# Performance work log

Hardware: AMD Instinct MI355X
Metric: run time of the kernel (lower is better)

Reference implementation:

```python
import jax, jax.numpy as jnp
import numpy as np
import math

V, T, E, H, L = 32000, 1024, 1024, 16, 6
B = 2
D = E // H
F = 4 * E


def setup_inputs() -> dict:
    key = jax.random.key(0)
    ks = jax.random.split(key, 12)
    s = 0.02
    rn = lambda k, shape: jax.random.normal(k, shape, jnp.float32) * s
    return dict(
        idx=jax.random.randint(ks[0], (B, T), 0, V),
        tok_w=rn(ks[1], (V, E)),
        pos_w=rn(ks[2], (T, E)),
        ln1_g=jnp.ones((L, E)), ln1_b=jnp.zeros((L, E)),
        wq=rn(ks[3], (L, E, E)), wk=rn(ks[4], (L, E, E)), wv=rn(ks[5], (L, E, E)),
        wp=rn(ks[6], (L, E, E)), bp=jnp.zeros((L, E)),
        ln2_g=jnp.ones((L, E)), ln2_b=jnp.zeros((L, E)),
        w1=rn(ks[7], (L, E, F)), b1=jnp.zeros((L, F)),
        w2=rn(ks[8], (L, F, E)), b2=jnp.zeros((L, E)),
        lnf_g=jnp.ones((E,)), lnf_b=jnp.zeros((E,)),
        wlm=rn(ks[9], (E, V)), blm=jnp.zeros((V,)),
    )


def _layernorm(x, g, b, eps=1e-5):
    m = jnp.mean(x, axis=-1, keepdims=True)
    v = jnp.var(x, axis=-1, keepdims=True)
    return (x - m) * jax.lax.rsqrt(v + eps) * g + b


def _forward(idx, tok_w, pos_w, ln1_g, ln1_b, wq, wk, wv, wp, bp,
             ln2_g, ln2_b, w1, b1, w2, b2, lnf_g, lnf_b, wlm, blm):
    Bx, Tx = idx.shape
    x = tok_w[idx] + pos_w[jnp.arange(Tx)][None, :, :]  # [B,T,E]
    causal = jnp.tril(jnp.ones((Tx, Tx), dtype=bool))
    scale = 1.0 / math.sqrt(D)
    for l in range(L):
        h = _layernorm(x, ln1_g[l], ln1_b[l])
        q = (h @ wq[l]).reshape(Bx, Tx, H, D).transpose(0, 2, 1, 3)  # [B,H,T,D]
        k = (h @ wk[l]).reshape(Bx, Tx, H, D).transpose(0, 2, 1, 3)
        v = (h @ wv[l]).reshape(Bx, Tx, H, D).transpose(0, 2, 1, 3)
        att = jnp.einsum('bhtd,bhsd->bhts', q, k) * scale  # [B,H,T,T]
        att = jnp.where(causal, att, -jnp.inf)
        att = jax.nn.softmax(att, axis=-1)
        y = jnp.einsum('bhts,bhsd->bhtd', att, v)
        y = y.transpose(0, 2, 1, 3).reshape(Bx, Tx, E)
        x = x + y @ wp[l] + bp[l]
        h2 = _layernorm(x, ln2_g[l], ln2_b[l])
        ff = jax.nn.gelu(h2 @ w1[l] + b1[l], approximate=False) @ w2[l] + b2[l]
        x = x + ff
    x = _layernorm(x, lnf_g, lnf_b)
    return x @ wlm + blm  # logits [B,T,V]


def reference(idx, tok_w, pos_w, ln1_g, ln1_b, wq, wk, wv, wp, bp,
              ln2_g, ln2_b, w1, b1, w2, b2, lnf_g, lnf_b, wlm, blm):
    return _forward(idx, tok_w, pos_w, ln1_g, ln1_b, wq, wk, wv, wp, bp,
                    ln2_g, ln2_b, w1, b1, w2, b2, lnf_g, lnf_b, wlm, blm)
```

## Files before the change

kernel.cpp:

```cpp
#include <hip/hip_runtime.h>

#define T_SEQ   1024
#define E_DIM   1024
#define H_HEADS 16
#define D_HEAD  64
#define L_LAYERS 6
#define B_BATCH 2
#define F_DIM   4096
#define V_VOCAB 32000

typedef float f32x4 __attribute__((ext_vector_type(4)));
typedef short short8 __attribute__((ext_vector_type(8)));

__device__ __forceinline__ unsigned short f2bf(float f) {
  union { float f; unsigned int u; } v; v.f = f;
  unsigned int r = v.u + 0x7fffu + ((v.u >> 16) & 1u);
  return (unsigned short)(r >> 16);
}

#define GLDS16(gp, lp) __builtin_amdgcn_global_load_lds( \
    (const __attribute__((address_space(1))) void*)(gp), \
    (__attribute__((address_space(3))) void*)(lp), 16, 0, 0)

__global__ void embed_kernel(const int* __restrict__ idx, const float* __restrict__ tok,
                             const float* __restrict__ pos, float* __restrict__ x) {
  int i = blockIdx.x * 256 + threadIdx.x;
  int bt = i >> 8;
  int e4 = i & 255;
  int t  = bt & (T_SEQ - 1);
  int tokid = idx[bt];
  f32x4 a = *(const f32x4*)(tok + (size_t)tokid * E_DIM + e4 * 4);
  f32x4 p = *(const f32x4*)(pos + (size_t)t * E_DIM + e4 * 4);
  *(f32x4*)(x + (size_t)bt * E_DIM + e4 * 4) = a + p;
}

__device__ __forceinline__ void ln_body(const float* __restrict__ x,
    const float* __restrict__ g, const float* __restrict__ b,
    unsigned short* __restrict__ out, int row) {
  int tid = threadIdx.x;
  const float* xr = x + (size_t)row * E_DIM;
  f32x4 v = *(const f32x4*)(xr + tid * 4);
  float s  = v[0] + v[1] + v[2] + v[3];
  float s2 = v[0]*v[0] + v[1]*v[1] + v[2]*v[2] + v[3]*v[3];
  #pragma unroll
  for (int off = 32; off > 0; off >>= 1) {
    s  += __shfl_xor(s,  off);
    s2 += __shfl_xor(s2, off);
  }
  __shared__ float red[2][4];
  int wave = tid >> 6;
  if ((tid & 63) == 0) { red[0][wave] = s; red[1][wave] = s2; }
  __syncthreads();
  s  = red[0][0] + red[0][1] + red[0][2] + red[0][3];
  s2 = red[1][0] + red[1][1] + red[1][2] + red[1][3];
  float mean = s * (1.0f / E_DIM);
  float var  = s2 * (1.0f / E_DIM) - mean * mean;
  float rstd = rsqrtf(var + 1e-5f);
  f32x4 gv = *(const f32x4*)(g + tid * 4);
  f32x4 bv = *(const f32x4*)(b + tid * 4);
  ushort4 o;
  o.x = f2bf((v[0] - mean) * rstd * gv[0] + bv[0]);
  o.y = f2bf((v[1] - mean) * rstd * gv[1] + bv[1]);
  o.z = f2bf((v[2] - mean) * rstd * gv[2] + bv[2]);
  o.w = f2bf((v[3] - mean) * rstd * gv[3] + bv[3]);
  *(ushort4*)(out + (size_t)row * E_DIM + tid * 4) = o;
}

__global__ void ln_kernel(const float* __restrict__ x, const float* __restrict__ g,
                          const float* __restrict__ b, unsigned short* __restrict__ out) {
  ln_body(x, g, b, out, blockIdx.x);
}

__device__ __forceinline__ void wtrans_body(const float* __restrict__ W,
    unsigned short* __restrict__ Wt, int K, int N, int bx, int by) {
  __shared__ float tile[64][65];
  const int n0 = bx * 64, k0 = by * 64;
  const int tr  = threadIdx.x >> 4;
  const int tc4 = (threadIdx.x & 15) * 4;
  #pragma unroll
  for (int p = 0; p < 4; ++p) {
    f32x4 v = *(const f32x4*)(W + (size_t)(k0 + p * 16 + tr) * N + n0 + tc4);
    tile[p * 16 + tr][tc4 + 0] = v[0];
    tile[p * 16 + tr][tc4 + 1] = v[1];
    tile[p * 16 + tr][tc4 + 2] = v[2];
    tile[p * 16 + tr][tc4 + 3] = v[3];
  }
  __syncthreads();
  #pragma unroll
  for (int p = 0; p < 4; ++p) {
    int n = p * 16 + tr;
    ushort4 o;
    o.x = f2bf(tile[tc4 + 0][n]);
    o.y = f2bf(tile[tc4 + 1][n]);
    o.z = f2bf(tile[tc4 + 2][n]);
    o.w = f2bf(tile[tc4 + 3][n]);
    *(ushort4*)(Wt + (size_t)(n0 + n) * K + k0 + tc4) = o;
  }
}

__global__ __launch_bounds__(256) void wtrans6ln_kernel(const float* __restrict__ wq,
    const float* __restrict__ wk, const float* __restrict__ wv, const float* __restrict__ wp,
    const float* __restrict__ w1, const float* __restrict__ w2,
    const float* __restrict__ lng, const float* __restrict__ lnb,
    const float* __restrict__ x, unsigned short* __restrict__ wtb,
    unsigned short* __restrict__ hb) {
  const size_t EE = (size_t)E_DIM * E_DIM;
  const size_t EF = (size_t)E_DIM * F_DIM;
  const int id = blockIdx.x;
  if (id < 1024) {
    const int z = id >> 8, r = id & 255;
    const float* W = z == 0 ? wq : (z == 1 ? wk : (z == 2 ? wv : wp));
    wtrans_body(W, wtb + z * EE, E_DIM, E_DIM, r & 15, r >> 4);
  } else if (id < 2048) {
    const int r = id - 1024;
    wtrans_body(w1, wtb + 4 * EE, E_DIM, F_DIM, r & 63, r >> 6);
  } else if (id < 3072) {
    const int r = id - 2048;
    wtrans_body(w2, wtb + 4 * EE + EF, F_DIM, E_DIM, r & 15, r >> 4);
  } else {
    ln_body(x, lng, lnb, hb, id - 3072);
  }
}

__global__ __launch_bounds__(256) void wtransv_ln_kernel(const float* __restrict__ wlm,
    const float* __restrict__ lng, const float* __restrict__ lnb,
    const float* __restrict__ x, unsigned short* __restrict__ wtb,
    unsigned short* __restrict__ hb) {
  const int id = blockIdx.x;
  if (id < 8000) wtrans_body(wlm, wtb, E_DIM, V_VOCAB, id % 500, id / 500);
  else           ln_body(x, lng, lnb, hb, id - 8000);
}

__global__ __launch_bounds__(512) void attn_mfma_kernel(
    const unsigned short* __restrict__ qk, const unsigned short* __restrict__ vt,
    unsigned short* __restrict__ y) {
  __shared__ __align__(16) char smem[2 * 16384 + 8 * 1280 + 512];
  const int tid  = threadIdx.x;
  const int lane = tid & 63;
  const int wave = tid >> 6;
  const int wl = wave & 3;
  const int g  = wave >> 2;
  const int qx = blockIdx.x;
  const int h  = blockIdx.y & (H_HEADS - 1);
  const int b  = blockIdx.y >> 4;
  const int qt = b ? (15 - qx) : qx;
  const int r0 = qt * 64 + wl * 16;
  const size_t RS = 2 * E_DIM;
  const unsigned short* q  = qk + (size_t)b * T_SEQ * RS + (size_t)h * D_HEAD;
  const unsigned short* k  = q + E_DIM;
  const unsigned short* vb = vt + (size_t)(b * H_HEADS + h) * D_HEAD * T_SEQ;
  const size_t ybase = (size_t)b * T_SEQ * E_DIM + (size_t)h * D_HEAD;
  const int fr = lane & 15, fg = lane >> 4;
  const int srow = lane >> 3;
  const int ssw  = ((lane & 7) * 16) ^ (srow << 4);
  char* pb = smem + 32768 + wave * 1280;
  float* mlb = (float*)(smem + 32768 + 10240);

  short8 aq[2];
  #pragma unroll
  for (int c = 0; c < 2; ++c)
    aq[c] = *(const short8*)(q + (size_t)(r0 + fr) * RS + c * 32 + fg * 8);

  f32x4 oacc[4];
  #pragma unroll
  for (int cg = 0; cg < 4; ++cg) oacc[cg] = (f32x4){0.f, 0.f, 0.f, 0.f};
  float m_ = -1e30f, l_ = 0.0f;

  auto stage = [&](int t) {
    const int j0 = t * 64;
    char* Kd = smem + (t & 1) * 16384;
    GLDS16((const char*)k  + (size_t)(j0 + wave * 8 + srow) * RS * 2 + ssw,
           Kd + wave * 1024);
    GLDS16((const char*)vb + ((size_t)(wave * 8 + srow) * T_SEQ + j0) * 2 + ssw,
           Kd + 8192 + wave * 1024);
  };

  stage(0);
  for (int t = 0; t <= qt; ++t) {
    __builtin_amdgcn_sched_barrier(0);
    __builtin_amdgcn_s_barrier();
    if (t < qt) stage(t + 1);
    __builtin_amdgcn_sched_barrier(0);
    if (t < qt) asm volatile("s_waitcnt vmcnt(2)" ::: "memory");
    else        asm volatile("s_waitcnt vmcnt(0)" ::: "memory");
    __builtin_amdgcn_sched_barrier(0);
    __builtin_amdgcn_s_barrier();
    __builtin_amdgcn_sched_barrier(0);
    const char* Kl = smem + (t & 1) * 16384;
    const char* Vl = Kl + 8192;
    const int j0 = t * 64;
    if (!(t == qt && g == 1 && wl < 2)) {
      f32x4 st[2];
      #pragma unroll
      for (int cc = 0; cc < 2; ++cc) {
        const int kloc = g * 32 + cc * 16 + fr;
        const char* kb = Kl + kloc * 128;
        const int sw = (kloc & 7) << 4;
        short8 ka0 = *(const short8*)(kb + ((fg * 16) ^ sw));
        short8 ka1 = *(const short8*)(kb + ((64 + fg * 16) ^ sw));
        f32x4 z = (f32x4){0.f, 0.f, 0.f, 0.f};
        z = __builtin_amdgcn_mfma_f32_16x16x32_bf16(ka0, aq[0], z, 0, 0, 0);
        z = __builtin_amdgcn_mfma_f32_16x16x32_bf16(ka1, aq[1], z, 0, 0, 0);
        st[cc] = z;
      }
      const int qg = r0 + fr;
      float pv[2][4];
      float mx = -1e30f;
      #pragma unroll
      for (int cc = 0; cc < 2; ++cc)
        #pragma unroll
        for (int r = 0; r < 4; ++r) {
          const int kj = j0 + g * 32 + cc * 16 + fg * 4 + r;
          float val = (kj <= qg) ? st[cc][r] * 0.125f : -1e30f;
          pv[cc][r] = val;
          mx = fmaxf(mx, val);
        }
      mx = fmaxf(mx, __shfl_xor(mx, 16));
      mx = fmaxf(mx, __shfl_xor(mx, 32));
      const float mn = fmaxf(m_, mx);
      const float cfs = __expf(m_ - mn);
      float ls = 0.0f;
      #pragma unroll
      for (int cc = 0; cc < 2; ++cc) {
        ushort4 o;
        float e0 = pv[cc][0] > -1e29f ? __expf(pv[cc][0] - mn) : 0.0f;
        float e1 = pv[cc][1] > -1e29f ? __expf(pv[cc][1] - mn) : 0.0f;
        float e2 = pv[cc][2] > -1e29f ? __expf(pv[cc][2] - mn) : 0.0f;
        float e3 = pv[cc][3] > -1e29f ? __expf(pv[cc][3] - mn) : 0.0f;
        ls += (e0 + e1) + (e2 + e3);
        o.x = f2bf(e0); o.y = f2bf(e1); o.z = f2bf(e2); o.w = f2bf(e3);
        *(ushort4*)(pb + fr * 80 + cc * 32 + fg * 8) = o;
      }
      ls += __shfl_xor(ls, 16);
      ls += __shfl_xor(ls, 32);
      l_ = l_ * cfs + ls;
      m_ = mn;
      float cfO[4];
      #pragma unroll
      for (int r = 0; r < 4; ++r) cfO[r] = __shfl(cfs, (lane & 48) | (fg * 4 + r));
      asm volatile("s_waitcnt lgkmcnt(0)" ::: "memory");
      __builtin_amdgcn_sched_barrier(0);
      short8 pa = *(const short8*)(pb + fr * 80 + fg * 16);
      __builtin_amdgcn_s_setprio(1);
      #pragma unroll
      for (int cg = 0; cg < 4; ++cg) {
        const int d = cg * 16 + fr;
        short8 bv = *(const short8*)(Vl + d * 128 + ((g * 64 + fg * 16) ^ ((d & 7) << 4)));
        #pragma unroll
        for (int r = 0; r < 4; ++r) oacc[cg][r] *= cfO[r];
        oacc[cg] = __builtin_amdgcn_mfma_f32_16x16x32_bf16(pa, bv, oacc[cg], 0, 0, 0);
      }
      __builtin_amdgcn_s_setprio(0);
    }
  }
  __syncthreads();
  float* obuf = (float*)smem;
  if (g == 1) {
    #pragma unroll
    for (int cg = 0; cg < 4; ++cg)
      #pragma unroll
      for (int r = 0; r < 4; ++r)
        obuf[wl * 1024 + (fg * 4 + r) * 64 + cg * 16 + fr] = oacc[cg][r];
    if (fg == 0) { mlb[(wl * 16 + fr) * 2] = m_; mlb[(wl * 16 + fr) * 2 + 1] = l_; }
  }
  __syncthreads();
  if (g == 0) {
    const float m1 = mlb[(wl * 16 + fr) * 2];
    const float l1 = mlb[(wl * 16 + fr) * 2 + 1];
    const float m  = fmaxf(m_, m1);
    const float c0 = __expf(m_ - m), c1 = __expf(m1 - m);
    const float li = 1.0f / (l_ * c0 + l1 * c1);
    float c0O[4], c1O[4], liO[4];
    #pragma unroll
    for (int r = 0; r < 4; ++r) {
      const int src = (lane & 48) | (fg * 4 + r);
      c0O[r] = __shfl(c0, src); c1O[r] = __shfl(c1, src); liO[r] = __shfl(li, src);
    }
    #pragma unroll
    for (int cg = 0; cg < 4; ++cg)
      #pragma unroll
      for (int r = 0; r < 4; ++r) {
        const float o1 = obuf[wl * 1024 + (fg * 4 + r) * 64 + cg * 16 + fr];
        const float val = (oacc[cg][r] * c0O[r] + o1 * c1O[r]) * liO[r];
        y[ybase + (size_t)(r0 + fg * 4 + r) * E_DIM + cg * 16 + fr] = f2bf(val);
      }
  }
}

template<int BM, int BN, bool HAS_BIAS, bool GELU_ACT, bool HAS_RES, int OMODE>
__global__ __launch_bounds__(256) void gemm_bt_kernel(
    const unsigned short* __restrict__ A, const unsigned short* __restrict__ Bt,
    const float* __restrict__ bias, const float* __restrict__ res,
    void* __restrict__ out, unsigned short* __restrict__ vt, int M, int N, int K) {
  constexpr int BK = 64;
  constexpr int MR = BM / 32;
  constexpr int NR = BN / 32;
  constexpr int AI = BM / 32;
  constexpr int BI = BN / 32;
  __shared__ __align__(16) char smem[(BM + BN) * BK * 2];
  unsigned short* As = (unsigned short*)smem;
  unsigned short* Bs = (unsigned short*)(smem + (size_t)BM * BK * 2);
  const int tid  = threadIdx.x;
  const int lane = tid & 63;
  const int wave = tid >> 6;
  const int wr = wave >> 1, wc = wave & 1;

  const int mt = M / BM;
  const int q8 = gridDim.x >> 3;
  const int g  = (blockIdx.x & 7) * q8 + (blockIdx.x >> 3);
  const int m0 = (g % mt) * BM, n0 = (g / mt) * BN;

  const int fr = lane & 15, fg = lane >> 4;
  const int lrow = lane >> 3;
  const int scol = ((lane & 7) * 16) ^ (lrow << 4);
  const size_t K2 = (size_t)K * 2;
  const char* aG = (const char*)A  + (size_t)(m0 + wave * 8 + lrow) * K2 + scol;
  const char* bG = (const char*)Bt + (size_t)(n0 + wave * 8 + lrow) * K2 + scol;

  f32x4 acc[MR][NR];
  #pragma unroll
  for (int mi = 0; mi < MR; ++mi)
    #pragma unroll
    for (int ni = 0; ni < NR; ++ni) acc[mi][ni] = (f32x4){0.f, 0.f, 0.f, 0.f};

  for (int k0 = 0; k0 < K; k0 += BK) {
    __syncthreads();
    #pragma unroll
    for (int i = 0; i < AI; ++i)
      GLDS16(aG + (size_t)i * 32 * K2 + (size_t)k0 * 2, (char*)As + wave * 1024 + i * 4096);
    #pragma unroll
    for (int i = 0; i < BI; ++i)
      GLDS16(bG + (size_t)i * 32 * K2 + (size_t)k0 * 2, (char*)Bs + wave * 1024 + i * 4096);
    __syncthreads();

    short8 af[MR][2], bf[NR][2];
    #pragma unroll
    for (int mi = 0; mi < MR; ++mi) {
      const int row = wr * (BM / 2) + mi * 16 + fr;
      #pragma unroll
      for (int kh = 0; kh < 2; ++kh)
        af[mi][kh] = *(const short8*)((const char*)As + row * 128 +
                       ((kh * 64 + fg * 16) ^ ((row & 7) << 4)));
    }
    #pragma unroll
    for (int ni = 0; ni < NR; ++ni) {
      const int row = wc * (BN / 2) + ni * 16 + fr;
      #pragma unroll
      for (int kh = 0; kh < 2; ++kh)
        bf[ni][kh] = *(const short8*)((const char*)Bs + row * 128 +
                       ((kh * 64 + fg * 16) ^ ((row & 7) << 4)));
    }
    #pragma unroll
    for (int mi = 0; mi < MR; ++mi)
      #pragma unroll
      for (int ni = 0; ni < NR; ++ni) {
        acc[mi][ni] = __builtin_amdgcn_mfma_f32_16x16x32_bf16(af[mi][0], bf[ni][0], acc[mi][ni], 0, 0, 0);
        acc[mi][ni] = __builtin_amdgcn_mfma_f32_16x16x32_bf16(af[mi][1], bf[ni][1], acc[mi][ni], 0, 0, 0);
      }
  }

  if (OMODE == 0) {
    __syncthreads();
    float* tw = (float*)(smem + wave * 4352);
    float bv4[NR];
    #pragma unroll
    for (int ni = 0; ni < NR; ++ni)
      bv4[ni] = HAS_BIAS ? bias[n0 + wc * (BN / 2) + ni * 16 + fr] : 0.0f;
    #pragma unroll
    for (int mi = 0; mi < MR; ++mi) {
      #pragma unroll
      for (int ni = 0; ni < NR; ++ni)
        #pragma unroll
        for (int r = 0; r < 4; ++r) {
          float val = acc[mi][ni][r] + bv4[ni];
          if (GELU_ACT) val = 0.5f * val * (1.0f + erff(val * 0.70710678118f));
          tw[(fg * 4 + r) * 68 + ni * 16 + fr] = val;
        }
      asm volatile("s_waitcnt lgkmcnt(0)" ::: "memory");
      __builtin_amdgcn_sched_barrier(0);
      #pragma unroll
      for (int rr = 0; rr < 4; ++rr) {
        const int row = rr * 4 + (lane >> 4);
        const int grow = m0 + wr * (BM / 2) + mi * 16 + row;
        const int gcol = n0 + wc * (BN / 2) + (lane & 15) * 4;
        f32x4 v = *(const f32x4*)&tw[row * 68 + (lane & 15) * 4];
        if (HAS_RES) v += *(const f32x4*)(res + (size_t)grow * N + gcol);
        *(f32x4*)((float*)out + (size_t)grow * N + gcol) = v;
      }
      asm volatile("s_waitcnt lgkmcnt(0)" ::: "memory");
      __builtin_amdgcn_sched_barrier(0);
    }
  } else {
    #pragma unroll
    for (int mi = 0; mi < MR; ++mi)
      #pragma unroll
      for (int ni = 0; ni < NR; ++ni) {
        const int col = n0 + wc * (BN / 2) + ni * 16 + fr;
        float bv = HAS_BIAS ? bias[col] : 0.0f;
        const int rbase = m0 + wr * (BM / 2) + mi * 16 + fg * 4;
        #pragma unroll
        for (int r = 0; r < 4; ++r) {
          float val = acc[mi][ni][r] + bv;
          if (GELU_ACT) val = 0.5f * val * (1.0f + erff(val * 0.70710678118f));
          ((unsigned short*)out)[(size_t)(rbase + r) * N + col] = f2bf(val);
        }
      }
  }
}

template<int OMODE, bool HAS_BIAS, bool GELU_ACT>
__global__ __launch_bounds__(512, 1) void gemm8p2_kernel(
    const unsigned short* __restrict__ A, const unsigned short* __restrict__ Bt,
    const float* __restrict__ bias, void* __restrict__ out,
    unsigned short* __restrict__ vt, int M, int N, int K) {
  __shared__ __align__(16) char lds[98304];
  const int tid  = threadIdx.x;
  const int lane = tid & 63;
  const int wv   = tid >> 6;
  const int wm = wv >> 2, wn = wv & 3;

  const int mt = M >> 7;
  const int q8 = gridDim.x >> 3;
  const int g  = (blockIdx.x & 7) * q8 + (blockIdx.x >> 3);
  const int m0 = (g % mt) * 128, n0 = (g / mt) * 256;

  const int fr = lane & 15, fg = lane >> 4;
  const size_t K2 = (size_t)K * 2;
  const int nIter = K >> 7;

  const int csw0 = (fg * 16) ^ ((fr & 7) << 4);
  const int csw1 = (64 + fg * 16) ^ ((fr & 7) << 4);

  const int sc = (lane * 16) & 127;
  const size_t laneoff = (size_t)(lane >> 3) * K2 + (size_t)(sc ^ ((lane >> 3) << 4));
  const char* Asrc = (const char*)(A + (size_t)m0 * K) + laneoff;
  const char* Bsrc = (const char*)(Bt + (size_t)n0 * K) + laneoff;
  const int arow_wv = (wv >> 2) * 64 + (wv & 3) * 8;
  const int brow_wv = (wv >> 2) * 64 + (wv & 3) * 8;

  f32x4 acc[4][4];
  #pragma unroll
  for (int i = 0; i < 4; ++i)
    #pragma unroll
    for (int j = 0; j < 4; ++j) acc[i][j] = (f32x4){0.f, 0.f, 0.f, 0.f};

  auto stageA = [&](int b, int c, int kt) {
    GLDS16(Asrc + (size_t)(arow_wv + c * 32) * K2 + (size_t)kt * 128,
           lds + b * 49152 + c * 8192 + wv * 1024);
  };
  auto stageB = [&](int b, int j, int kt) {
    GLDS16(Bsrc + (size_t)((j & 1) * 128 + (j >> 1) * 32 + brow_wv) * K2 + (size_t)kt * 128,
           lds + b * 49152 + 16384 + j * 8192 + wv * 1024);
  };

  stageA(0, 0, 0); stageA(0, 1, 0);
  stageB(0, 0, 0); stageB(0, 1, 0); stageB(0, 2, 0); stageB(0, 3, 0);
  stageA(1, 0, 1); stageB(1, 0, 1); stageB(1, 1, 1);
  __builtin_amdgcn_sched_barrier(0);
  asm volatile("s_waitcnt vmcnt(3)" ::: "memory");
  __builtin_amdgcn_s_barrier();

  for (int i = 0; i < nIter; ++i) {
    const bool last = (i == nIter - 1);
    #pragma unroll
    for (int p = 0; p < 8; ++p) {
      const int b  = p >> 2;
      const int mh = (p >> 1) & 1;
      const int nh = p & 1;
      const char* Ab = lds + b * 49152;
      const char* Bb = Ab + 16384;
      __builtin_amdgcn_sched_barrier(0);
      short8 fa[2][2], fb[2][2];
      #pragma unroll
      for (int j = 0; j < 2; ++j) {
        const int row = mh * 64 + wm * 32 + j * 16 + fr;
        fa[j][0] = *(const short8*)(Ab + row * 128 + csw0);
        fa[j][1] = *(const short8*)(Ab + row * 128 + csw1);
      }
      #pragma unroll
      for (int n = 0; n < 2; ++n) {
        const int row = nh * 128 + (wn >> 1) * 64 + (wn & 1) * 32 + n * 16 + fr;
        fb[n][0] = *(const short8*)(Bb + row * 128 + csw0);
        fb[n][1] = *(const short8*)(Bb + row * 128 + csw1);
      }
      if (p == 0) stageA(1, 1, 2 * i + 1);
      if (p == 1) { stageB(1, 2, 2 * i + 1); stageB(1, 3, 2 * i + 1); }
      if (!last) {
        if (p == 2) stageA(0, 0, 2 * i + 2);
        if (p == 3) { stageB(0, 0, 2 * i + 2); stageB(0, 1, 2 * i + 2); }
        if (p == 4) stageA(0, 1, 2 * i + 2);
        if (p == 5) { stageB(0, 2, 2 * i + 2); stageB(0, 3, 2 * i + 2); }
        if (p == 6) stageA(1, 0, 2 * i + 3);
        if (p == 7) { stageB(1, 0, 2 * i + 3); stageB(1, 1, 2 * i + 3); }
      }
      __builtin_amdgcn_sched_barrier(0);
      __builtin_amdgcn_s_barrier();
      __builtin_amdgcn_sched_barrier(0);
      __builtin_amdgcn_s_setprio(1);
      #pragma unroll
      for (int j = 0; j < 2; ++j)
        #pragma unroll
        for (int n = 0; n < 2; ++n) {
          acc[mh * 2 + j][nh * 2 + n] = __builtin_amdgcn_mfma_f32_16x16x32_bf16(
              fa[j][0], fb[n][0], acc[mh * 2 + j][nh * 2 + n], 0, 0, 0);
          acc[mh * 2 + j][nh * 2 + n] = __builtin_amdgcn_mfma_f32_16x16x32_bf16(
              fa[j][1], fb[n][1], acc[mh * 2 + j][nh * 2 + n], 0, 0, 0);
        }
      __builtin_amdgcn_s_setprio(0);
      __builtin_amdgcn_sched_barrier(0);
      if (p == 3) {
        if (!last) asm volatile("s_waitcnt vmcnt(3)" ::: "memory");
        else       asm volatile("s_waitcnt vmcnt(0)" ::: "memory");
      }
      if (p == 7 && !last)
        asm volatile("s_waitcnt vmcnt(3)" ::: "memory");
      __builtin_amdgcn_s_barrier();
    }
  }

  if (OMODE == 1) {
    unsigned short* tw = (unsigned short*)(lds + wv * 2176);
    float bv4[4];
    #pragma unroll
    for (int ni = 0; ni < 4; ++ni)
      bv4[ni] = HAS_BIAS ? bias[n0 + wn * 64 + ni * 16 + fr] : 0.0f;
    #pragma unroll
    for (int mi = 0; mi < 4; ++mi) {
      #pragma unroll
      for (int ni = 0; ni < 4; ++ni)
        #pragma unroll
        for (int r = 0; r < 4; ++r) {
          float val = acc[mi][ni][r] + bv4[ni];
          if (GELU_ACT) val = 0.5f * val * (1.0f + erff(val * 0.70710678118f));
          tw[(fg * 4 + r) * 68 + ni * 16 + fr] = f2bf(val);
        }
      asm volatile("s_waitcnt lgkmcnt(0)" ::: "memory");
      __builtin_amdgcn_sched_barrier(0);
      #pragma unroll
      for (int rr = 0; rr < 4; ++rr) {
        const int row = rr * 4 + (lane >> 4);
        const int grow = m0 + wm * 64 + mi * 16 + row;
        const int gcol = n0 + wn * 64 + (lane & 15) * 4;
        ushort4 v = *(const ushort4*)&tw[row * 68 + (lane & 15) * 4];
        *(ushort4*)((unsigned short*)out + (size_t)grow * N + gcol) = v;
      }
      asm volatile("s_waitcnt lgkmcnt(0)" ::: "memory");
      __builtin_amdgcn_sched_barrier(0);
    }
  } else {
    #pragma unroll
    for (int mi = 0; mi < 4; ++mi) {
      #pragma unroll
      for (int ni = 0; ni < 4; ++ni) {
        const int col = n0 + wn * 64 + ni * 16 + fr;
        float bv = HAS_BIAS ? bias[col] : 0.0f;
        const int rbase = m0 + wm * 64 + mi * 16 + fg * 4;
        float vals[4];
        #pragma unroll
        for (int r = 0; r < 4; ++r) vals[r] = acc[mi][ni][r] + bv;
        if (col < 2 * E_DIM) {
          #pragma unroll
          for (int r = 0; r < 4; ++r)
            ((unsigned short*)out)[(size_t)(rbase + r) * 2 * E_DIM + col] = f2bf(vals[r]);
        } else {
          const int c2 = col - 2 * E_DIM;
          const int hh = c2 >> 6, d = c2 & 63;
          const int bb = rbase >> 10, t0 = rbase & (T_SEQ - 1);
          ushort4 o;
          o.x = f2bf(vals[0]); o.y = f2bf(vals[1]);
          o.z = f2bf(vals[2]); o.w = f2bf(vals[3]);
          *(ushort4*)(vt + ((size_t)(bb * H_HEADS + hh) * D_HEAD + d) * T_SEQ + t0) = o;
        }
      }
    }
  }
}

__global__ __launch_bounds__(512, 1) void gemm8p_kernel(
    const unsigned short* __restrict__ A, const unsigned short* __restrict__ Bt,
    const float* __restrict__ bias, float* __restrict__ out, int M, int N, int K) {
  __shared__ __align__(16) char lds[131072];
  const int tid  = threadIdx.x;
  const int lane = tid & 63;
  const int wv   = tid >> 6;
  const int wm = wv >> 2, wn = wv & 3;

  const int mt = M >> 8;
  const int q8 = gridDim.x >> 3;
  const int g  = (blockIdx.x & 7) * q8 + (blockIdx.x >> 3);
  const int m0 = (g % mt) * 256, n0 = (g / mt) * 256;

  const int fr = lane & 15, fg = lane >> 4;
  const size_t K2 = (size_t)K * 2;
  const int nIter = K >> 7;

  const int csw0 = (fg * 16) ^ ((fr & 7) << 4);
  const int csw1 = (64 + fg * 16) ^ ((fr & 7) << 4);

  const int sc = (lane * 16) & 127;
  const size_t laneoff = (size_t)(lane >> 3) * K2 + (size_t)(sc ^ ((lane >> 3) << 4));
  const char* Asrc = (const char*)(A + (size_t)m0 * K) + (size_t)(wv * 8) * K2 + laneoff;
  const char* Bsrc = (const char*)(Bt + (size_t)n0 * K) + laneoff;

  f32x4 acc[8][4];
  #pragma unroll
  for (int i = 0; i < 8; ++i)
    #pragma unroll
    for (int j = 0; j < 4; ++j) acc[i][j] = (f32x4){0.f, 0.f, 0.f, 0.f};

  auto stageA = [&](int b, int q, int kt) {
    GLDS16(Asrc + (size_t)(q * 64) * K2 + (size_t)kt * 128,
           lds + b * 65536 + q * 8192 + wv * 1024);
  };
  auto stageB = [&](int b, int j, int o, int kt) {
    const int gw = j * 64 + wv * 8;
    const int rw = ((gw >> 5) << 6) + (gw & 31) + o * 32;
    GLDS16(Bsrc + (size_t)rw * K2 + (size_t)kt * 128,
           lds + b * 65536 + 32768 + rw * 128);
  };

  stageA(0, 0, 0); stageA(0, 2, 0);
  stageB(0, 0, 0, 0); stageB(0, 1, 0, 0);
  stageA(0, 1, 0); stageA(0, 3, 0);
  stageB(0, 0, 1, 0); stageB(0, 1, 1, 0);
  stageA(1, 0, 1); stageA(1, 2, 1);
  stageB(1, 0, 0, 1); stageB(1, 1, 0, 1);
  __builtin_amdgcn_sched_barrier(0);
  asm volatile("s_waitcnt vmcnt(4)" ::: "memory");
  __builtin_amdgcn_s_barrier();

  for (int i = 0; i < nIter; ++i) {
    const bool last = (i == nIter - 1);
    #pragma unroll
    for (int p = 0; p < 8; ++p) {
      const int b  = p >> 2;
      const int mh = (p & 3) >> 1;
      const int nh = p & 1;
      const char* Ab = lds + b * 65536;
      const char* Bb = Ab + 32768;
      __builtin_amdgcn_sched_barrier(0);
      short8 fa[4][2], fb[2][2];
      #pragma unroll
      for (int j = 0; j < 4; ++j) {
        const int row = wm * 128 + mh * 64 + j * 16 + fr;
        fa[j][0] = *(const short8*)(Ab + row * 128 + csw0);
        fa[j][1] = *(const short8*)(Ab + row * 128 + csw1);
      }
      #pragma unroll
      for (int n = 0; n < 2; ++n) {
        const int row = wn * 64 + nh * 32 + n * 16 + fr;
        fb[n][0] = *(const short8*)(Bb + row * 128 + csw0);
        fb[n][1] = *(const short8*)(Bb + row * 128 + csw1);
      }
      if (p == 0) { stageA(1, 1, 2 * i + 1); stageA(1, 3, 2 * i + 1); }
      if (p == 1) { stageB(1, 0, 1, 2 * i + 1); stageB(1, 1, 1, 2 * i + 1); }
      if (!last) {
        if (p == 2) { stageA(0, 0, 2 * i + 2); stageA(0, 2, 2 * i + 2); }
        if (p == 3) { stageB(0, 0, 0, 2 * i + 2); stageB(0, 1, 0, 2 * i + 2); }
        if (p == 4) { stageA(0, 1, 2 * i + 2); stageA(0, 3, 2 * i + 2); }
        if (p == 5) { stageB(0, 0, 1, 2 * i + 2); stageB(0, 1, 1, 2 * i + 2); }
        if (p == 6) { stageA(1, 0, 2 * i + 3); stageA(1, 2, 2 * i + 3); }
        if (p == 7) { stageB(1, 0, 0, 2 * i + 3); stageB(1, 1, 0, 2 * i + 3); }
      }
      __builtin_amdgcn_sched_barrier(0);
      __builtin_amdgcn_s_barrier();
      __builtin_amdgcn_sched_barrier(0);
      __builtin_amdgcn_s_setprio(1);
      #pragma unroll
      for (int j = 0; j < 4; ++j)
        #pragma unroll
        for (int n = 0; n < 2; ++n) {
          acc[mh * 4 + j][nh * 2 + n] = __builtin_amdgcn_mfma_f32_16x16x32_bf16(
              fa[j][0], fb[n][0], acc[mh * 4 + j][nh * 2 + n], 0, 0, 0);
          acc[mh * 4 + j][nh * 2 + n] = __builtin_amdgcn_mfma_f32_16x16x32_bf16(
              fa[j][1], fb[n][1], acc[mh * 4 + j][nh * 2 + n], 0, 0, 0);
        }
      __builtin_amdgcn_s_setprio(0);
      __builtin_amdgcn_sched_barrier(0);
      if (p == 3) {
        if (!last) asm volatile("s_waitcnt vmcnt(4)" ::: "memory");
        else       asm volatile("s_waitcnt vmcnt(0)" ::: "memory");
      }
      if (p == 7 && !last)
        asm volatile("s_waitcnt vmcnt(4)" ::: "memory");
      __builtin_amdgcn_s_barrier();
    }
  }

  float* tw = (float*)(lds + wv * 4352);
  float bv4[4];
  #pragma unroll
  for (int ni = 0; ni < 4; ++ni) bv4[ni] = bias[n0 + wn * 64 + ni * 16 + fr];
  #pragma unroll
  for (int mi = 0; mi < 8; ++mi) {
    #pragma unroll
    for (int ni = 0; ni < 4; ++ni)
      #pragma unroll
      for (int r = 0; r < 4; ++r)
        tw[(fg * 4 + r) * 68 + ni * 16 + fr] = acc[mi][ni][r] + bv4[ni];
    asm volatile("s_waitcnt lgkmcnt(0)" ::: "memory");
    __builtin_amdgcn_sched_barrier(0);
    #pragma unroll
    for (int rr = 0; rr < 4; ++rr) {
      const int row = rr * 4 + (lane >> 4);
      const int grow = m0 + wm * 128 + mi * 16 + row;
      const int gcol = n0 + wn * 64 + (lane & 15) * 4;
      f32x4 v = *(const f32x4*)&tw[row * 68 + (lane & 15) * 4];
      *(f32x4*)(out + (size_t)grow * N + gcol) = v;
    }
    asm volatile("s_waitcnt lgkmcnt(0)" ::: "memory");
    __builtin_amdgcn_sched_barrier(0);
  }
}

extern "C" void kernel_launch(void* const* d_in, const int* in_sizes, int n_in,
                              void* d_out, int out_size, void* d_ws, size_t ws_size,
                              hipStream_t stream) {
  const int*   idx   = (const int*)  d_in[0];
  const float* tok_w = (const float*)d_in[1];
  const float* pos_w = (const float*)d_in[2];
  const float* ln1_g = (const float*)d_in[3];
  const float* ln1_b = (const float*)d_in[4];
  const float* wq    = (const float*)d_in[5];
  const float* wk    = (const float*)d_in[6];
  const float* wv    = (const float*)d_in[7];
  const float* wp    = (const float*)d_in[8];
  const float* bp    = (const float*)d_in[9];
  const float* ln2_g = (const float*)d_in[10];
  const float* ln2_b = (const float*)d_in[11];
  const float* w1    = (const float*)d_in[12];
  const float* b1    = (const float*)d_in[13];
  const float* w2    = (const float*)d_in[14];
  const float* b2    = (const float*)d_in[15];
  const float* lnf_g = (const float*)d_in[16];
  const float* lnf_b = (const float*)d_in[17];
  const float* wlm   = (const float*)d_in[18];
  const float* blm   = (const float*)d_in[19];

  const int M = B_BATCH * T_SEQ;
  const size_t EE = (size_t)E_DIM * E_DIM;
  const size_t EF = (size_t)E_DIM * F_DIM;
  char* p = (char*)d_ws;
  float* x            = (float*)p;          p += (size_t)M * E_DIM * 4;
  unsigned short* hb  = (unsigned short*)p; p += (size_t)M * E_DIM * 2;
  unsigned short* qkb = (unsigned short*)p; p += (size_t)M * 2 * E_DIM * 2;
  unsigned short* vtb = (unsigned short*)p; p += (size_t)M * E_DIM * 2;
  unsigned short* yb  = (unsigned short*)p; p += (size_t)M * E_DIM * 2;
  unsigned short* tb  = (unsigned short*)p; p += (size_t)M * F_DIM * 2;
  unsigned short* wtb = (unsigned short*)p; p += (size_t)V_VOCAB * E_DIM * 2;

  embed_kernel<<<M * E_DIM / 4 / 256, 256, 0, stream>>>(idx, tok_w, pos_w, x);

  for (int l = 0; l < L_LAYERS; ++l) {
    wtrans6ln_kernel<<<5120, 256, 0, stream>>>(
        wq + l * EE, wk + l * EE, wv + l * EE, wp + l * EE,
        w1 + l * EF, w2 + l * EF,
        ln1_g + (size_t)l * E_DIM, ln1_b + (size_t)l * E_DIM, x, wtb, hb);
    gemm8p2_kernel<2, false, false>
        <<<(M / 128) * (3 * E_DIM / 256), 512, 0, stream>>>(
        hb, wtb, nullptr, qkb, vtb, M, 3 * E_DIM, E_DIM);
    attn_mfma_kernel<<<dim3(16, B_BATCH * H_HEADS), 512, 0, stream>>>(qkb, vtb, yb);
    gemm_bt_kernel<64, 128, true, false, true, 0>
        <<<(M / 64) * (E_DIM / 128), 256, 0, stream>>>(
        yb, wtb + 3 * EE, bp + (size_t)l * E_DIM, x, x, nullptr, M, E_DIM, E_DIM);
    ln_kernel<<<M, 256, 0, stream>>>(x, ln2_g + (size_t)l * E_DIM, ln2_b + (size_t)l * E_DIM, hb);
    gemm8p2_kernel<1, true, true>
        <<<(M / 128) * (F_DIM / 256), 512, 0, stream>>>(
        hb, wtb + 4 * EE, b1 + (size_t)l * F_DIM, tb, nullptr, M, F_DIM, E_DIM);
    gemm_bt_kernel<64, 128, true, false, true, 0>
        <<<(M / 64) * (E_DIM / 128), 256, 0, stream>>>(
        tb, wtb + 4 * EE + EF, b2 + (size_t)l * E_DIM, x, x, nullptr, M, E_DIM, F_DIM);
  }
  wtransv_ln_kernel<<<10048, 256, 0, stream>>>(wlm, lnf_g, lnf_b, x, wtb, hb);
  gemm8p_kernel<<<(M / 256) * (V_VOCAB / 256), 512, 0, stream>>>(
      hb, wtb, blm, (float*)d_out, M, V_VOCAB, E_DIM);
}
```

Baseline: 1.292 ms.

## Make LM-head GEMM persistent with cross-tile prefetch and direct epilogue stores

Launches the vocab-projection GEMM with a fixed 256-block persistent grid. Each block walks its XCD-local tiles with stride 32 and prefetches the next tile's first K-slices during the last iteration of the current tile, so the pipeline does not drain and refill between tiles. Because LDS is still holding the prefetched data, the epilogue now writes bias-added accumulators straight to global memory instead of staging them through LDS. That risks less coalesced stores on the large logits output.

```diff
diff --git a/kernel.cpp b/kernel.cpp
--- a/kernel.cpp
+++ b/kernel.cpp
@@ -584,23 +584,34 @@
   const int lane = tid & 63;
   const int wv   = tid >> 6;
   const int wm = wv >> 2, wn = wv & 3;
-
-  const int mt = M >> 8;
-  const int q8 = gridDim.x >> 3;
-  const int g  = (blockIdx.x & 7) * q8 + (blockIdx.x >> 3);
-  const int m0 = (g % mt) * 256, n0 = (g / mt) * 256;
-
   const int fr = lane & 15, fg = lane >> 4;
   const size_t K2 = (size_t)K * 2;
   const int nIter = K >> 7;
+  const int mt = M >> 8;
+  const int perX = (mt * (N >> 8)) >> 3;
+  const int xcd = blockIdx.x & 7, local = blockIdx.x >> 3;
 
   const int csw0 = (fg * 16) ^ ((fr & 7) << 4);
   const int csw1 = (64 + fg * 16) ^ ((fr & 7) << 4);
-
   const int sc = (lane * 16) & 127;
   const size_t laneoff = (size_t)(lane >> 3) * K2 + (size_t)(sc ^ ((lane >> 3) << 4));
-  const char* Asrc = (const char*)(A + (size_t)m0 * K) + (size_t)(wv * 8) * K2 + laneoff;
-  const char* Bsrc = (const char*)(Bt + (size_t)n0 * K) + laneoff;
+
+  auto srcA = [&](int g) {
+    return (const char*)(A + (size_t)((g % mt) * 256) * K) + (size_t)(wv * 8) * K2 + laneoff;
+  };
+  auto srcB = [&](int g) {
+    return (const char*)(Bt + (size_t)((g / mt) * 256) * K) + laneoff;
+  };
+  auto stageA = [&](const char* S, int b, int q, int kt) {
+    GLDS16(S + (size_t)(q * 64) * K2 + (size_t)kt * 128,
+           lds + b * 65536 + q * 8192 + wv * 1024);
+  };
+  auto stageB = [&](const char* S, int b, int j, int o, int kt) {
+    const int gw = j * 64 + wv * 8;
+    const int rw = ((gw >> 5) << 6) + (gw & 31) + o * 32;
+    GLDS16(S + (size_t)rw * K2 + (size_t)kt * 128,
+           lds + b * 65536 + 32768 + rw * 128);
+  };
 
   f32x4 acc[8][4];
   #pragma unroll
@@ -608,108 +619,105 @@
     #pragma unroll
     for (int j = 0; j < 4; ++j) acc[i][j] = (f32x4){0.f, 0.f, 0.f, 0.f};
 
-  auto stageA = [&](int b, int q, int kt) {
-    GLDS16(Asrc + (size_t)(q * 64) * K2 + (size_t)kt * 128,
-           lds + b * 65536 + q * 8192 + wv * 1024);
-  };
-  auto stageB = [&](int b, int j, int o, int kt) {
-    const int gw = j * 64 + wv * 8;
-    const int rw = ((gw >> 5) << 6) + (gw & 31) + o * 32;
-    GLDS16(Bsrc + (size_t)rw * K2 + (size_t)kt * 128,
-           lds + b * 65536 + 32768 + rw * 128);
-  };
-
-  stageA(0, 0, 0); stageA(0, 2, 0);
-  stageB(0, 0, 0, 0); stageB(0, 1, 0, 0);
-  stageA(0, 1, 0); stageA(0, 3, 0);
-  stageB(0, 0, 1, 0); stageB(0, 1, 1, 0);
-  stageA(1, 0, 1); stageA(1, 2, 1);
-  stageB(1, 0, 0, 1); stageB(1, 1, 0, 1);
+  int g = xcd * perX + local;
+  const char* Ac = srcA(g);
+  const char* Bc = srcB(g);
+
+  stageA(Ac, 0, 0, 0); stageA(Ac, 0, 2, 0);
+  stageB(Bc, 0, 0, 0, 0); stageB(Bc, 0, 1, 0, 0);
+  stageA(Ac, 0, 1, 0); stageA(Ac, 0, 3, 0);
+  stageB(Bc, 0, 0, 1, 0); stageB(Bc, 0, 1, 1, 0);
+  stageA(Ac, 1, 0, 1); stageA(Ac, 1, 2, 1);
+  stageB(Bc, 1, 0, 0, 1); stageB(Bc, 1, 1, 0, 1);
   __builtin_amdgcn_sched_barrier(0);
   asm volatile("s_waitcnt vmcnt(4)" ::: "memory");
   __builtin_amdgcn_s_barrier();
 
-  for (int i = 0; i < nIter; ++i) {
-    const bool last = (i == nIter - 1);
-    #pragma unroll
-    for (int p = 0; p < 8; ++p) {
-      const int b  = p >> 2;
-      const int mh = (p & 3) >> 1;
-      const int nh = p & 1;
-      const char* Ab = lds + b * 65536;
-      const char* Bb = Ab + 32768;
-      __builtin_amdgcn_sched_barrier(0);
-      short8 fa[4][2], fb[2][2];
-      #pragma unroll
-      for (int j = 0; j < 4; ++j) {
-        const int row = wm * 128 + mh * 64 + j * 16 + fr;
-        fa[j][0] = *(const short8*)(Ab + row * 128 + csw0);
-        fa[j][1] = *(const short8*)(Ab + row * 128 + csw1);
-      }
-      #pragma unroll
-      for (int n = 0; n < 2; ++n) {
-        const int row = wn * 64 + nh * 32 + n * 16 + fr;
-        fb[n][0] = *(const short8*)(Bb + row * 128 + csw0);
-        fb[n][1] = *(const short8*)(Bb + row * 128 + csw1);
-      }
-      if (p == 0) { stageA(1, 1, 2 * i + 1); stageA(1, 3, 2 * i + 1); }
-      if (p == 1) { stageB(1, 0, 1, 2 * i + 1); stageB(1, 1, 1, 2 * i + 1); }
-      if (!last) {
-        if (p == 2) { stageA(0, 0, 2 * i + 2); stageA(0, 2, 2 * i + 2); }
-        if (p == 3) { stageB(0, 0, 0, 2 * i + 2); stageB(0, 1, 0, 2 * i + 2); }
-        if (p == 4) { stageA(0, 1, 2 * i + 2); stageA(0, 3, 2 * i + 2); }
-        if (p == 5) { stageB(0, 0, 1, 2 * i + 2); stageB(0, 1, 1, 2 * i + 2); }
-        if (p == 6) { stageA(1, 0, 2 * i + 3); stageA(1, 2, 2 * i + 3); }
-        if (p == 7) { stageB(1, 0, 0, 2 * i + 3); stageB(1, 1, 0, 2 * i + 3); }
-      }
-      __builtin_amdgcn_sched_barrier(0);
-      __builtin_amdgcn_s_barrier();
-      __builtin_amdgcn_sched_barrier(0);
-      __builtin_amdgcn_s_setprio(1);
-      #pragma unroll
-      for (int j = 0; j < 4; ++j)
+  for (int w = local; w < perX; w += 32) {
+    const bool finalW = (w + 32 >= perX);
+    const int gN = finalW ? g : (g + 32);
+    const char* An = srcA(gN);
+    const char* Bn = srcB(gN);
+    const int m0 = (g % mt) * 256, n0 = (g / mt) * 256;
+
+    for (int i = 0; i < nIter; ++i) {
+      const bool wrap = (i == nIter - 1);
+      const bool skip = wrap && finalW;
+      const char* Aw = wrap ? An : Ac;
+      const char* Bw = wrap ? Bn : Bc;
+      const int kt2 = wrap ? 0 : (2 * i + 2);
+      const int kt3 = wrap ? 1 : (2 * i + 3);
+      #pragma unroll
+      for (int p = 0; p < 8; ++p) {
+        const int b  = p >> 2;
+        const int mh = (p & 3) >> 1;
+        const int nh = p & 1;
+        const char* Ab = lds + b * 65536;
+        const char* Bb = Ab + 32768;
+        __builtin_amdgcn_sched_barrier(0);
+        short8 fa[4][2], fb[2][2];
+        #pragma unroll
+        for (int j = 0; j < 4; ++j) {
+          const int row = wm * 128 + mh * 64 + j * 16 + fr;
+          fa[j][0] = *(const short8*)(Ab + row * 128 + csw0);
+          fa[j][1] = *(const short8*)(Ab + row * 128 + csw1);
+        }
         #pragma unroll
         for (int n = 0; n < 2; ++n) {
-          acc[mh * 4 + j][nh * 2 + n] = __builtin_amdgcn_mfma_f32_16x16x32_bf16(
-              fa[j][0], fb[n][0], acc[mh * 4 + j][nh * 2 + n], 0, 0, 0);
-          acc[mh * 4 + j][nh * 2 + n] = __builtin_amdgcn_mfma_f32_16x16x32_bf16(
-              fa[j][1], fb[n][1], acc[mh * 4 + j][nh * 2 + n], 0, 0, 0);
-        }
-      __builtin_amdgcn_s_setprio(0);
-      __builtin_amdgcn_sched_barrier(0);
-      if (p == 3) {
-        if (!last) asm volatile("s_waitcnt vmcnt(4)" ::: "memory");
-        else       asm volatile("s_waitcnt vmcnt(0)" ::: "memory");
-      }
-      if (p == 7 && !last)
-        asm volatile("s_waitcnt vmcnt(4)" ::: "memory");
-      __builtin_amdgcn_s_barrier();
-    }
-  }
-
-  float* tw = (float*)(lds + wv * 4352);
-  float bv4[4];
-  #pragma unroll
-  for (int ni = 0; ni < 4; ++ni) bv4[ni] = bias[n0 + wn * 64 + ni * 16 + fr];
-  #pragma unroll
-  for (int mi = 0; mi < 8; ++mi) {
-    #pragma unroll
-    for (int ni = 0; ni < 4; ++ni)
-      #pragma unroll
-      for (int r = 0; r < 4; ++r)
-        tw[(fg * 4 + r) * 68 + ni * 16 + fr] = acc[mi][ni][r] + bv4[ni];
-    asm volatile("s_waitcnt lgkmcnt(0)" ::: "memory");
-    __builtin_amdgcn_sched_barrier(0);
-    #pragma unroll
-    for (int rr = 0; rr < 4; ++rr) {
-      const int row = rr * 4 + (lane >> 4);
-      const int grow = m0 + wm * 128 + mi * 16 + row;
-      const int gcol = n0 + wn * 64 + (lane & 15) * 4;
-      f32x4 v = *(const f32x4*)&tw[row * 68 + (lane & 15) * 4];
-      *(f32x4*)(out + (size_t)grow * N + gcol) = v;
-    }
-    asm volatile("s_waitcnt lgkmcnt(0)" ::: "memory");
-    __builtin_amdgcn_sched_barrier(0);
+          const int row = wn * 64 + nh * 32 + n * 16 + fr;
+          fb[n][0] = *(const short8*)(Bb + row * 128 + csw0);
+          fb[n][1] = *(const short8*)(Bb + row * 128 + csw1);
+        }
+        if (p == 0) { stageA(Ac, 1, 1, 2 * i + 1); stageA(Ac, 1, 3, 2 * i + 1); }
+        if (p == 1) { stageB(Bc, 1, 0, 1, 2 * i + 1); stageB(Bc, 1, 1, 1, 2 * i + 1); }
+        if (!skip) {
+          if (p == 2) { stageA(Aw, 0, 0, kt2); stageA(Aw, 0, 2, kt2); }
+          if (p == 3) { stageB(Bw, 0, 0, 0, kt2); stageB(Bw, 0, 1, 0, kt2); }
+          if (p == 4) { stageA(Aw, 0, 1, kt2); stageA(Aw, 0, 3, kt2); }
+          if (p == 5) { stageB(Bw, 0, 0, 1, kt2); stageB(Bw, 0, 1, 1, kt2); }
+          if (p == 6) { stageA(Aw, 1, 0, kt3); stageA(Aw, 1, 2, kt3); }
+          if (p == 7) { stageB(Bw, 1, 0, 0, kt3); stageB(Bw, 1, 1, 0, kt3); }
+        }
+        __builtin_amdgcn_sched_barrier(0);
+        __builtin_amdgcn_s_barrier();
+        __builtin_amdgcn_sched_barrier(0);
+        __builtin_amdgcn_s_setprio(1);
+        #pragma unroll
+        for (int j = 0; j < 4; ++j)
+          #pragma unroll
+          for (int n = 0; n < 2; ++n) {
+            acc[mh * 4 + j][nh * 2 + n] = __builtin_amdgcn_mfma_f32_16x16x32_bf16(
+                fa[j][0], fb[n][0], acc[mh * 4 + j][nh * 2 + n], 0, 0, 0);
+            acc[mh * 4 + j][nh * 2 + n] = __builtin_amdgcn_mfma_f32_16x16x32_bf16(
+                fa[j][1], fb[n][1], acc[mh * 4 + j][nh * 2 + n], 0, 0, 0);
+          }
+        __builtin_amdgcn_s_setprio(0);
+        __builtin_amdgcn_sched_barrier(0);
+        if (p == 3) {
+          if (!skip) asm volatile("s_waitcnt vmcnt(4)" ::: "memory");
+          else       asm volatile("s_waitcnt vmcnt(0)" ::: "memory");
+        }
+        if (p == 7 && !skip)
+          asm volatile("s_waitcnt vmcnt(4)" ::: "memory");
+        __builtin_amdgcn_s_barrier();
+      }
+    }
+
+    #pragma unroll
+    for (int mi = 0; mi < 8; ++mi) {
+      #pragma unroll
+      for (int ni = 0; ni < 4; ++ni) {
+        const int col = n0 + wn * 64 + ni * 16 + fr;
+        const float bv = bias[col];
+        #pragma unroll
+        for (int r = 0; r < 4; ++r) {
+          const int row = m0 + wm * 128 + mi * 16 + fg * 4 + r;
+          out[(size_t)row * N + col] = acc[mi][ni][r] + bv;
+          acc[mi][ni][r] = 0.0f;
+        }
+      }
+    }
+    g = gN; Ac = An; Bc = Bn;
   }
 }
 
@@ -772,6 +780,6 @@
         tb, wtb + 4 * EE + EF, b2 + (size_t)l * E_DIM, x, x, nullptr, M, E_DIM, F_DIM);
   }
   wtransv_ln_kernel<<<10048, 256, 0, stream>>>(wlm, lnf_g, lnf_b, x, wtb, hb);
-  gemm8p_kernel<<<(M / 256) * (V_VOCAB / 256), 512, 0, stream>>>(
+  gemm8p_kernel<<<256, 512, 0, stream>>>(
       hb, wtb, blm, (float*)d_out, M, V_VOCAB, E_DIM);
 }
```

After: 1.305 ms. Within noise of the previous version (+1.0%).
